# Kernel optimization log

Hardware: AMD Instinct MI355X
Metric: run time of the kernel (lower is better)

The kernel has to match this reference:

```python
import jax, jax.numpy as jnp
import numpy as np

M, N, DIM = 128, 128, 256
BS = 8192
START_SIGMA = max(M, N) / 2.0
EPOCHS = 20.0
START_LR = 0.5
TAU = EPOCHS / np.log(START_SIGMA)


def setup_inputs() -> dict:
    key = jax.random.key(0)
    k_data, k_w = jax.random.split(key)
    data = jax.random.normal(k_data, (BS, DIM), dtype=jnp.float32)
    all_weights = jax.random.normal(k_w, (M, N, DIM), dtype=jnp.float32)
    return {"data": data, "all_weights": all_weights, "it": 3}


def reference(data, all_weights, it):
    m, n, dim = all_weights.shape
    bs = data.shape[0]

    # decayed sigma and learning rate (scalar schedule)
    sigma = START_SIGMA * jnp.exp(-jnp.float32(it) / jnp.float32(TAU))
    lr = START_LR * jnp.exp(-jnp.float32(it) / jnp.float32(EPOCHS))

    # pairwise Euclidean distances: [bs, m*n]
    w_flat = all_weights.reshape(m * n, dim)
    x_sq = jnp.sum(data * data, axis=1, keepdims=True)            # [bs, 1]
    w_sq = jnp.sum(w_flat * w_flat, axis=1)[None, :]              # [1, m*n]
    dists = jnp.sqrt(x_sq + w_sq - 2.0 * data @ w_flat.T)         # [bs, m*n]

    # best-matching unit grid coordinates (unravel over (m, n))
    bmu = jnp.argmin(dists, axis=1)                               # [bs]
    wins0 = (bmu // n).astype(jnp.float32)                        # row coord
    wins1 = (bmu % n).astype(jnp.float32)                         # col coord

    # Gaussian neighborhood around BMU, scaled by lr: [bs, m, n]
    d = 2.0 * sigma * sigma
    rows = jnp.arange(m, dtype=jnp.float32)
    cols = jnp.arange(n, dtype=jnp.float32)
    px = jnp.exp(-(rows[None, :] - wins0[:, None]) ** 2 / d)      # [bs, m]
    py = jnp.exp(-(cols[None, :] - wins1[:, None]) ** 2 / d)      # [bs, n]
    neighbor = (px[:, :, None] * py[:, None, :]) * lr             # [bs, m, n]

    # weighted batch update of the codebook
    denom = jnp.sum(neighbor, axis=0)[..., None]                  # [m, n, 1]
    numer = jnp.einsum('bk,bd->kd', neighbor.reshape(bs, m * n), data)
    numer = numer.reshape(m, n, dim)                              # [m, n, dim]
    new_weights = jnp.where(denom != 0, numer / denom, all_weights)
    return new_weights
```

## Files before the change

kernel.cpp:

```cpp
#include <hip/hip_runtime.h>
#include <hip/hip_fp16.h>

#define BS    8192
#define DIM   256
#define KTOT  16384
#define CAND_CAP 131072
#define MARGIN 1.0f

typedef __attribute__((ext_vector_type(8))) _Float16 half8;
typedef __attribute__((ext_vector_type(4))) float f32x4;
typedef unsigned long long u64;

__device__ inline ushort f2h(float f) { return __half_as_ushort(__float2half(f)); }

__device__ inline void gload_lds16(const void* g, void* l) {
    __builtin_amdgcn_global_load_lds(
        (const __attribute__((address_space(1))) unsigned int*)g,
        (__attribute__((address_space(3))) unsigned int*)l, 16, 0, 0);
}

__device__ inline unsigned int fmap(float f) {
    unsigned int b = __float_as_uint(f);
    return (b & 0x80000000u) ? ~b : (b | 0x80000000u);
}
__device__ inline float unfmap(unsigned int m) {
    return (m & 0x80000000u) ? __uint_as_float(m & 0x7FFFFFFFu)
                             : __uint_as_float(~m);
}

__global__ void setup_all_kernel(float* __restrict__ S, float* __restrict__ G,
                                 float* __restrict__ cntf, unsigned int* __restrict__ keys,
                                 u64* __restrict__ keys2, unsigned int* __restrict__ cnt,
                                 const int* __restrict__ itp) {
    int idx = blockIdx.x * 256 + threadIdx.x;
    *(float4*)&S[(size_t)idx * 4] = make_float4(0.f, 0.f, 0.f, 0.f);
    if (idx < KTOT) {
        float itf = (float)itp[0];
        const float START_SIGMA = 64.0f;
        const float TAU = (float)(20.0 / 4.1588830833596715);
        float sigma = START_SIGMA * expf(-itf / TAU);
        float d2 = 2.0f * sigma * sigma;
        int i = idx >> 7, j = idx & 127;
        float diff = (float)(i - j);
        G[idx] = expf(-(diff * diff) / d2);
        cntf[idx] = 0.f;
    }
    if (idx < BS) { keys[idx] = 0xFFFFFFFFu; keys2[idx] = ~0ULL; }
    if (idx == 0) cnt[0] = 0u;
}

__global__ void cvt_all_kernel(const float* __restrict__ x, const float* __restrict__ w,
                               ushort* __restrict__ xf, ushort* __restrict__ wf,
                               float* __restrict__ wsq) {
    int wid = threadIdx.x >> 6, lane = threadIdx.x & 63;
    int row = blockIdx.x * 4 + wid;
    int h = lane * 4;
    int window = h >> 5, c = (h >> 3) & 3, off = h & 7;
    if (row < BS) {
        int swpos = (window << 5) + (((c ^ ((row >> 1) & 3)) << 3)) + off;
        float4 v = *(const float4*)&x[(size_t)row * DIM + h];
        ushort4 hv;
        hv.x = f2h(v.x); hv.y = f2h(v.y); hv.z = f2h(v.z); hv.w = f2h(v.w);
        *(ushort4*)&xf[(size_t)row * DIM + swpos] = hv;
    } else {
        int r = row - BS;
        int swpos = (window << 5) + (((c ^ ((r >> 1) & 3)) << 3)) + off;
        float4 v = *(const float4*)&w[(size_t)r * DIM + h];
        ushort4 hv;
        hv.x = f2h(v.x); hv.y = f2h(v.y); hv.z = f2h(v.z); hv.w = f2h(v.w);
        *(ushort4*)&wf[(size_t)r * DIM + swpos] = hv;
        float s = v.x * v.x + v.y * v.y + v.z * v.z + v.w * v.w;
        #pragma unroll
        for (int o = 32; o; o >>= 1) s += __shfl_down(s, o, 64);
        if (lane == 0) wsq[r] = s;
    }
}

__global__ __launch_bounds__(256) void bmu_pass1_kernel(
    const ushort* __restrict__ xf, const ushort* __restrict__ wf,
    const float* __restrict__ wsq, unsigned int* __restrict__ keys) {
    __shared__ ushort A[128 * 32];
    __shared__ ushort B[128 * 32];
    __shared__ float red[128][2];

    int m0 = blockIdx.x * 128;
    int kbase = blockIdx.y * 1024;
    int tid = threadIdx.x, w = tid >> 6, lane = tid & 63;
    int wm = (w & 1) * 64, wn = (w >> 1) * 64;
    int lm = lane & 15, quad = lane >> 4;
    int sw = (quad ^ ((lm >> 1) & 3)) * 8;
    int srow = lane >> 2, scol = (lane & 3) * 8;

    float best[4][4];
    #pragma unroll
    for (int mi = 0; mi < 4; ++mi)
        #pragma unroll
        for (int r = 0; r < 4; ++r) best[mi][r] = 3.4e38f;

    for (int kt = 0; kt < 8; ++kt) {
        int k0 = kbase + kt * 128;
        f32x4 acc[4][4];
        #pragma unroll
        for (int mi = 0; mi < 4; ++mi)
            #pragma unroll
            for (int ni = 0; ni < 4; ++ni)
                acc[mi][ni] = (f32x4){0.f, 0.f, 0.f, 0.f};

        for (int kb = 0; kb < DIM; kb += 32) {
            size_t axoff = (size_t)(m0 + w * 32 + srow) * DIM + kb + scol;
            size_t bxoff = (size_t)(k0 + w * 32 + srow) * DIM + kb + scol;
            gload_lds16(xf + axoff,            &A[(w * 32) * 32]);
            gload_lds16(xf + axoff + 16 * DIM, &A[(w * 32 + 16) * 32]);
            gload_lds16(wf + bxoff,            &B[(w * 32) * 32]);
            gload_lds16(wf + bxoff + 16 * DIM, &B[(w * 32 + 16) * 32]);
            __syncthreads();
            half8 av[4], bv[4];
            #pragma unroll
            for (int mi = 0; mi < 4; ++mi)
                av[mi] = *(const half8*)&A[(wm + mi * 16 + lm) * 32 + sw];
            #pragma unroll
            for (int ni = 0; ni < 4; ++ni)
                bv[ni] = *(const half8*)&B[(wn + ni * 16 + lm) * 32 + sw];
            #pragma unroll
            for (int mi = 0; mi < 4; ++mi)
                #pragma unroll
                for (int ni = 0; ni < 4; ++ni)
                    acc[mi][ni] = __builtin_amdgcn_mfma_f32_16x16x32_f16(
                        av[mi], bv[ni], acc[mi][ni], 0, 0, 0);
            __syncthreads();
        }
        float wsqv[4];
        #pragma unroll
        for (int ni = 0; ni < 4; ++ni) wsqv[ni] = wsq[k0 + wn + ni * 16 + lm];
        #pragma unroll
        for (int mi = 0; mi < 4; ++mi)
            #pragma unroll
            for (int r = 0; r < 4; ++r) {
                #pragma unroll
                for (int ni = 0; ni < 4; ++ni) {
                    float sc = fmaf(-2.0f, acc[mi][ni][r], wsqv[ni]);
                    best[mi][r] = fminf(best[mi][r], sc);
                }
            }
    }
    #pragma unroll
    for (int mi = 0; mi < 4; ++mi)
        #pragma unroll
        for (int r = 0; r < 4; ++r) {
            float b = best[mi][r];
            #pragma unroll
            for (int mask = 1; mask < 16; mask <<= 1)
                b = fminf(b, __shfl_xor(b, mask, 64));
            if (lm == 0) red[wm + mi * 16 + quad * 4 + r][w >> 1] = b;
        }
    __syncthreads();
    if (tid < 128) {
        float b = fminf(red[tid][0], red[tid][1]);
        atomicMin(&keys[m0 + tid], fmap(b));
    }
}

__global__ __launch_bounds__(256) void bmu_pass2_kernel(
    const ushort* __restrict__ xf, const ushort* __restrict__ wf,
    const float* __restrict__ wsq, const unsigned int* __restrict__ keys,
    u64* __restrict__ cand, unsigned int* __restrict__ cnt) {
    __shared__ ushort A[128 * 32];
    __shared__ ushort B[128 * 32];

    int m0 = blockIdx.x * 128;
    int kbase = blockIdx.y * 1024;
    int tid = threadIdx.x, w = tid >> 6, lane = tid & 63;
    int wm = (w & 1) * 64, wn = (w >> 1) * 64;
    int lm = lane & 15, quad = lane >> 4;
    int sw = (quad ^ ((lm >> 1) & 3)) * 8;
    int srow = lane >> 2, scol = (lane & 3) * 8;

    float thr[4][4];
    #pragma unroll
    for (int mi = 0; mi < 4; ++mi)
        #pragma unroll
        for (int r = 0; r < 4; ++r)
            thr[mi][r] = unfmap(keys[m0 + wm + mi * 16 + quad * 4 + r]) + MARGIN;

    for (int kt = 0; kt < 8; ++kt) {
        int k0 = kbase + kt * 128;
        f32x4 acc[4][4];
        #pragma unroll
        for (int mi = 0; mi < 4; ++mi)
            #pragma unroll
            for (int ni = 0; ni < 4; ++ni)
                acc[mi][ni] = (f32x4){0.f, 0.f, 0.f, 0.f};

        for (int kb = 0; kb < DIM; kb += 32) {
            size_t axoff = (size_t)(m0 + w * 32 + srow) * DIM + kb + scol;
            size_t bxoff = (size_t)(k0 + w * 32 + srow) * DIM + kb + scol;
            gload_lds16(xf + axoff,            &A[(w * 32) * 32]);
            gload_lds16(xf + axoff + 16 * DIM, &A[(w * 32 + 16) * 32]);
            gload_lds16(wf + bxoff,            &B[(w * 32) * 32]);
            gload_lds16(wf + bxoff + 16 * DIM, &B[(w * 32 + 16) * 32]);
            __syncthreads();
            half8 av[4], bv[4];
            #pragma unroll
            for (int mi = 0; mi < 4; ++mi)
                av[mi] = *(const half8*)&A[(wm + mi * 16 + lm) * 32 + sw];
            #pragma unroll
            for (int ni = 0; ni < 4; ++ni)
                bv[ni] = *(const half8*)&B[(wn + ni * 16 + lm) * 32 + sw];
            #pragma unroll
            for (int mi = 0; mi < 4; ++mi)
                #pragma unroll
                for (int ni = 0; ni < 4; ++ni)
                    acc[mi][ni] = __builtin_amdgcn_mfma_f32_16x16x32_f16(
                        av[mi], bv[ni], acc[mi][ni], 0, 0, 0);
            __syncthreads();
        }
        float wsqv[4];
        #pragma unroll
        for (int ni = 0; ni < 4; ++ni) wsqv[ni] = wsq[k0 + wn + ni * 16 + lm];
        #pragma unroll
        for (int mi = 0; mi < 4; ++mi)
            #pragma unroll
            for (int r = 0; r < 4; ++r) {
                int s = m0 + wm + mi * 16 + quad * 4 + r;
                #pragma unroll
                for (int ni = 0; ni < 4; ++ni) {
                    float sc = fmaf(-2.0f, acc[mi][ni][r], wsqv[ni]);
                    if (sc <= thr[mi][r]) {
                        unsigned int idx = atomicAdd(cnt, 1u);
                        if (idx < CAND_CAP)
                            cand[idx] = ((u64)(unsigned int)s << 32) |
                                        (unsigned int)(k0 + wn + ni * 16 + lm);
                    }
                }
            }
    }
}

__global__ __launch_bounds__(256) void bmu_refine_kernel(
    const float* __restrict__ x, const float* __restrict__ w,
    const u64* __restrict__ cand, const unsigned int* __restrict__ cnt,
    u64* __restrict__ keys2) {
    int lane = threadIdx.x & 63;
    int wid = blockIdx.x * 4 + (threadIdx.x >> 6);
    unsigned int n = cnt[0];
    if (n > CAND_CAP) n = CAND_CAP;
    for (unsigned int c = wid; c < n; c += 256 * 4) {
        u64 e = cand[c];
        unsigned int s = (unsigned int)(e >> 32);
        unsigned int k = (unsigned int)e;
        float4 xv = *(const float4*)&x[(size_t)s * DIM + lane * 4];
        float4 wv = *(const float4*)&w[(size_t)k * DIM + lane * 4];
        float dx = xv.x - wv.x, dy = xv.y - wv.y;
        float dz = xv.z - wv.z, dw = xv.w - wv.w;
        float d = dx * dx + dy * dy + dz * dz + dw * dw;
        #pragma unroll
        for (int off = 32; off; off >>= 1) d += __shfl_down(d, off, 64);
        if (lane == 0)
            atomicMin(&keys2[s], ((u64)fmap(d) << 32) | k);
    }
}

__global__ __launch_bounds__(256) void scatter_kernel(
    const float* __restrict__ x, const u64* __restrict__ keys2,
    float* __restrict__ S, float* __restrict__ cntf) {
    int lane = threadIdx.x & 63;
    int s = blockIdx.x * 4 + (threadIdx.x >> 6);
    unsigned int k = (unsigned int)keys2[s];
    float4 xv = *(const float4*)&x[(size_t)s * DIM + lane * 4];
    float* Sp = &S[(size_t)k * DIM + lane * 4];
    atomicAdd(Sp + 0, xv.x);
    atomicAdd(Sp + 1, xv.y);
    atomicAdd(Sp + 2, xv.z);
    atomicAdd(Sp + 3, xv.w);
    if (lane == 0) atomicAdd(&cntf[k], 1.0f);
}

__global__ __launch_bounds__(256) void gemm1_kernel(
    const float* __restrict__ G, const float* __restrict__ S, float* __restrict__ T) {
    __shared__ float Sl[128 * 68];
    int n0 = blockIdx.x * 64;
    int tid = threadIdx.x;
    #pragma unroll
    for (int q = 0; q < 8; ++q) {
        int idx = q * 256 + tid;
        int row = idx >> 4, c4 = (idx & 15) * 4;
        *(float4*)&Sl[row * 68 + c4] = *(const float4*)&S[(size_t)row * 32768 + n0 + c4];
    }
    __syncthreads();
    int ng = tid & 15, ig = tid >> 4;
    for (int pass = 0; pass < 2; ++pass) {
        int ibase = pass * 64 + ig * 4;
        float acc[4][4] = {};
        for (int a = 0; a < 128; ++a) {
            float4 sv = *(const float4*)&Sl[a * 68 + ng * 4];
            #pragma unroll
            for (int ii = 0; ii < 4; ++ii) {
                float g = G[(ibase + ii) * 128 + a];
                acc[ii][0] = fmaf(g, sv.x, acc[ii][0]);
                acc[ii][1] = fmaf(g, sv.y, acc[ii][1]);
                acc[ii][2] = fmaf(g, sv.z, acc[ii][2]);
                acc[ii][3] = fmaf(g, sv.w, acc[ii][3]);
            }
        }
        #pragma unroll
        for (int ii = 0; ii < 4; ++ii)
            *(float4*)&T[(size_t)(ibase + ii) * 32768 + n0 + ng * 4] =
                *(float4*)&acc[ii][0];
    }
}

__global__ void denom_s1_kernel(const float* __restrict__ cntf, const float* __restrict__ G,
                                float* __restrict__ M1) {
    int a = blockIdx.x, j = threadIdx.x;
    float acc = 0.f;
    for (int b2 = 0; b2 < 128; ++b2)
        acc = fmaf(cntf[a * 128 + b2], G[b2 * 128 + j], acc);
    M1[a * 128 + j] = acc;
}

__global__ void denom_s2_kernel(const float* __restrict__ G, const float* __restrict__ M1,
                                float* __restrict__ denom) {
    int i = blockIdx.x, j = threadIdx.x;
    float acc = 0.f;
    for (int a = 0; a < 128; ++a)
        acc = fmaf(G[i * 128 + a], M1[a * 128 + j], acc);
    denom[i * 128 + j] = acc;
}

__global__ __launch_bounds__(256) void gemm2_fin_kernel(
    const float* __restrict__ G, const float* __restrict__ T,
    const float* __restrict__ denom, const float* __restrict__ w,
    float* __restrict__ out) {
    __shared__ float Tl[128 * 68];
    int i = blockIdx.x, dq = blockIdx.y;
    int tid = threadIdx.x;
    #pragma unroll
    for (int q = 0; q < 8; ++q) {
        int idx = q * 256 + tid;
        int row = idx >> 4, c4 = (idx & 15) * 4;
        *(float4*)&Tl[row * 68 + c4] =
            *(const float4*)&T[(size_t)i * 32768 + row * 256 + dq * 64 + c4];
    }
    __syncthreads();
    int dg = tid & 15, jg = tid >> 4;
    for (int pass = 0; pass < 2; ++pass) {
        int jbase = pass * 64 + jg * 4;
        float acc[4][4] = {};
        for (int b2 = 0; b2 < 128; ++b2) {
            float4 tv = *(const float4*)&Tl[b2 * 68 + dg * 4];
            #pragma unroll
            for (int jj = 0; jj < 4; ++jj) {
                float g = G[(jbase + jj) * 128 + b2];
                acc[jj][0] = fmaf(g, tv.x, acc[jj][0]);
                acc[jj][1] = fmaf(g, tv.y, acc[jj][1]);
                acc[jj][2] = fmaf(g, tv.z, acc[jj][2]);
                acc[jj][3] = fmaf(g, tv.w, acc[jj][3]);
            }
        }
        #pragma unroll
        for (int jj = 0; jj < 4; ++jj) {
            int j = jbase + jj;
            float dv = denom[i * 128 + j];
            size_t e = (size_t)(i * 128 + j) * DIM + dq * 64 + dg * 4;
            float4 r;
            if (dv != 0.0f) {
                float inv = 1.0f / dv;
                r.x = acc[jj][0] * inv; r.y = acc[jj][1] * inv;
                r.z = acc[jj][2] * inv; r.w = acc[jj][3] * inv;
            } else {
                r = *(const float4*)&w[e];
            }
            *(float4*)&out[e] = r;
        }
    }
}

extern "C" void kernel_launch(void* const* d_in, const int* in_sizes, int n_in,
                              void* d_out, int out_size, void* d_ws, size_t ws_size,
                              hipStream_t stream) {
    const float* data = (const float*)d_in[0];
    const float* w    = (const float*)d_in[1];
    const int*   itp  = (const int*)d_in[2];
    float* out = (float*)d_out;

    char* ws = (char*)d_ws;
    size_t off = 0;
    float*        wsq   = (float*)(ws + off);        off += 65536;
    unsigned int* keys  = (unsigned int*)(ws + off); off += 65536;
    u64*          keys2 = (u64*)(ws + off);          off += 65536;
    unsigned int* cnt   = (unsigned int*)(ws + off); off += 65536;
    float*        G     = (float*)(ws + off);        off += 65536;
    float*        cntf  = (float*)(ws + off);        off += 65536;
    float*        M1    = (float*)(ws + off);        off += 65536;
    float*        denom = (float*)(ws + off);        off += 65536;
    ushort*       xf    = (ushort*)(ws + off);       off += 4194304;
    ushort*       wf    = (ushort*)(ws + off);       off += 8388608;
    u64*          cand  = (u64*)(ws + off);          off += 1048576;
    float*        S     = (float*)(ws + off);        off += 16777216;
    float*        T     = (float*)(ws + off);        off += 16777216;

    setup_all_kernel<<<4096, 256, 0, stream>>>(S, G, cntf, keys, keys2, cnt, itp);
    cvt_all_kernel<<<(BS + KTOT) / 4, 256, 0, stream>>>(data, w, xf, wf, wsq);
    bmu_pass1_kernel<<<dim3(64, 16), 256, 0, stream>>>(xf, wf, wsq, keys);
    bmu_pass2_kernel<<<dim3(64, 16), 256, 0, stream>>>(xf, wf, wsq, keys, cand, cnt);
    bmu_refine_kernel<<<256, 256, 0, stream>>>(data, w, cand, cnt, keys2);
    scatter_kernel<<<BS / 4, 256, 0, stream>>>(data, keys2, S, cntf);
    gemm1_kernel<<<512, 256, 0, stream>>>(G, S, T);
    denom_s1_kernel<<<128, 128, 0, stream>>>(cntf, G, M1);
    denom_s2_kernel<<<128, 128, 0, stream>>>(G, M1, denom);
    gemm2_fin_kernel<<<dim3(128, 4), 256, 0, stream>>>(G, T, denom, w, out);
}
```

Before: 402.6 us.

## Replace two-pass BMU GEMM with single scan storing quantized per-lane minima

The two full fp16 distance GEMM passes (one for the min threshold, one to collect candidates) become a single scan. The scan writes a byte-quantized minimum for each group of four codebook columns into a 32MB buffer. A collect kernel finds each sample's quantized minimum and emits group tasks within a small margin, and a rescore kernel evaluates the 4 columns of each group exactly in fp32. The goal is to drop one of the two GEMM passes; the cost is extra global traffic for the byte buffer, a fixed quantization scale and offset that assume a particular score range, and a changed k-split grid (12 splits over 128 tiles).

Result: slower. 516.7 us (+28.4%).

```diff
diff --git a/kernel.cpp b/kernel.cpp
--- a/kernel.cpp
+++ b/kernel.cpp
@@ -4,8 +4,7 @@
 #define BS    8192
 #define DIM   256
 #define KTOT  16384
-#define CAND_CAP 131072
-#define MARGIN 1.0f
+#define TASK_CAP 131072
 
 typedef __attribute__((ext_vector_type(8))) _Float16 half8;
 typedef __attribute__((ext_vector_type(4))) float f32x4;
@@ -23,15 +22,10 @@
     unsigned int b = __float_as_uint(f);
     return (b & 0x80000000u) ? ~b : (b | 0x80000000u);
 }
-__device__ inline float unfmap(unsigned int m) {
-    return (m & 0x80000000u) ? __uint_as_float(m & 0x7FFFFFFFu)
-                             : __uint_as_float(~m);
-}
 
 __global__ void setup_all_kernel(float* __restrict__ S, float* __restrict__ G,
-                                 float* __restrict__ cntf, unsigned int* __restrict__ keys,
-                                 u64* __restrict__ keys2, unsigned int* __restrict__ cnt,
-                                 const int* __restrict__ itp) {
+                                 float* __restrict__ cntf, u64* __restrict__ keys2,
+                                 unsigned int* __restrict__ cnt, const int* __restrict__ itp) {
     int idx = blockIdx.x * 256 + threadIdx.x;
     *(float4*)&S[(size_t)idx * 4] = make_float4(0.f, 0.f, 0.f, 0.f);
     if (idx < KTOT) {
@@ -45,7 +39,7 @@
         G[idx] = expf(-(diff * diff) / d2);
         cntf[idx] = 0.f;
     }
-    if (idx < BS) { keys[idx] = 0xFFFFFFFFu; keys2[idx] = ~0ULL; }
+    if (idx < BS) keys2[idx] = ~0ULL;
     if (idx == 0) cnt[0] = 0u;
 }
 
@@ -57,14 +51,14 @@
     int h = lane * 4;
     int window = h >> 5, c = (h >> 3) & 3, off = h & 7;
     if (row < BS) {
-        int swpos = (window << 5) + (((c ^ ((row >> 1) & 3)) << 3)) + off;
+        int swpos = (window << 5) + ((c ^ ((row >> 1) & 3)) << 3) + off;
         float4 v = *(const float4*)&x[(size_t)row * DIM + h];
         ushort4 hv;
         hv.x = f2h(v.x); hv.y = f2h(v.y); hv.z = f2h(v.z); hv.w = f2h(v.w);
         *(ushort4*)&xf[(size_t)row * DIM + swpos] = hv;
     } else {
         int r = row - BS;
-        int swpos = (window << 5) + (((c ^ ((r >> 1) & 3)) << 3)) + off;
+        int swpos = (window << 5) + ((c ^ ((r >> 1) & 3)) << 3) + off;
         float4 v = *(const float4*)&w[(size_t)r * DIM + h];
         ushort4 hv;
         hv.x = f2h(v.x); hv.y = f2h(v.y); hv.z = f2h(v.z); hv.w = f2h(v.w);
@@ -76,29 +70,25 @@
     }
 }
 
-__global__ __launch_bounds__(256) void bmu_pass1_kernel(
+__global__ __launch_bounds__(256, 3) void bmu_scan_kernel(
     const ushort* __restrict__ xf, const ushort* __restrict__ wf,
-    const float* __restrict__ wsq, unsigned int* __restrict__ keys) {
+    const float* __restrict__ wsq, unsigned char* __restrict__ laneMin) {
     __shared__ ushort A[128 * 32];
     __shared__ ushort B[128 * 32];
-    __shared__ float red[128][2];
 
     int m0 = blockIdx.x * 128;
-    int kbase = blockIdx.y * 1024;
+    int ksplit = blockIdx.y;
     int tid = threadIdx.x, w = tid >> 6, lane = tid & 63;
-    int wm = (w & 1) * 64, wn = (w >> 1) * 64;
+    int wm = (w & 1) * 64;
+    int wnIdx = w >> 1, wn = wnIdx * 64;
     int lm = lane & 15, quad = lane >> 4;
     int sw = (quad ^ ((lm >> 1) & 3)) * 8;
     int srow = lane >> 2, scol = (lane & 3) * 8;
 
-    float best[4][4];
-    #pragma unroll
-    for (int mi = 0; mi < 4; ++mi)
-        #pragma unroll
-        for (int r = 0; r < 4; ++r) best[mi][r] = 3.4e38f;
-
-    for (int kt = 0; kt < 8; ++kt) {
-        int k0 = kbase + kt * 128;
+    for (int kt = 0; kt < 11; ++kt) {
+        int tile = kt * 12 + ksplit;
+        if (tile >= 128) break;
+        int k0 = tile * 128;
         f32x4 acc[4][4];
         #pragma unroll
         for (int mi = 0; mi < 4; ++mi)
@@ -132,131 +122,86 @@
         float wsqv[4];
         #pragma unroll
         for (int ni = 0; ni < 4; ++ni) wsqv[ni] = wsq[k0 + wn + ni * 16 + lm];
-        #pragma unroll
-        for (int mi = 0; mi < 4; ++mi)
+        size_t baseA = ((size_t)(tile * 2 + wnIdx) * 8192 + m0 + wm + quad * 4) * 16 + lm;
+        #pragma unroll
+        for (int mi = 0; mi < 4; ++mi) {
             #pragma unroll
             for (int r = 0; r < 4; ++r) {
-                #pragma unroll
-                for (int ni = 0; ni < 4; ++ni) {
-                    float sc = fmaf(-2.0f, acc[mi][ni][r], wsqv[ni]);
-                    best[mi][r] = fminf(best[mi][r], sc);
-                }
+                float s0 = fmaf(-2.0f, acc[mi][0][r], wsqv[0]);
+                float s1 = fmaf(-2.0f, acc[mi][1][r], wsqv[1]);
+                float s2 = fmaf(-2.0f, acc[mi][2][r], wsqv[2]);
+                float s3 = fmaf(-2.0f, acc[mi][3][r], wsqv[3]);
+                float m = fminf(fminf(s0, s1), fminf(s2, s3));
+                float qf = fminf(fmaxf(rintf(fmaf(m, 0.33333334f, 100.0f)), 0.f), 255.f);
+                laneMin[baseA + (size_t)(mi * 16 + r) * 16] = (unsigned char)(int)qf;
             }
+        }
+    }
+}
+
+__global__ __launch_bounds__(256) void collect_kernel(
+    const unsigned char* __restrict__ laneMin, unsigned int* __restrict__ tasks,
+    unsigned int* __restrict__ cnt) {
+    int tid = threadIdx.x;
+    int sl = tid >> 4, lm = tid & 15;
+    int s = blockIdx.x * 16 + sl;
+    int qmin = 255;
+    #pragma unroll 4
+    for (int t = 0; t < 256; ++t) {
+        int v = laneMin[((size_t)t * 8192 + s) * 16 + lm];
+        qmin = v < qmin ? v : qmin;
     }
     #pragma unroll
-    for (int mi = 0; mi < 4; ++mi)
-        #pragma unroll
-        for (int r = 0; r < 4; ++r) {
-            float b = best[mi][r];
-            #pragma unroll
-            for (int mask = 1; mask < 16; mask <<= 1)
-                b = fminf(b, __shfl_xor(b, mask, 64));
-            if (lm == 0) red[wm + mi * 16 + quad * 4 + r][w >> 1] = b;
-        }
-    __syncthreads();
-    if (tid < 128) {
-        float b = fminf(red[tid][0], red[tid][1]);
-        atomicMin(&keys[m0 + tid], fmap(b));
-    }
-}
-
-__global__ __launch_bounds__(256) void bmu_pass2_kernel(
-    const ushort* __restrict__ xf, const ushort* __restrict__ wf,
-    const float* __restrict__ wsq, const unsigned int* __restrict__ keys,
-    u64* __restrict__ cand, unsigned int* __restrict__ cnt) {
-    __shared__ ushort A[128 * 32];
-    __shared__ ushort B[128 * 32];
-
-    int m0 = blockIdx.x * 128;
-    int kbase = blockIdx.y * 1024;
-    int tid = threadIdx.x, w = tid >> 6, lane = tid & 63;
-    int wm = (w & 1) * 64, wn = (w >> 1) * 64;
-    int lm = lane & 15, quad = lane >> 4;
-    int sw = (quad ^ ((lm >> 1) & 3)) * 8;
-    int srow = lane >> 2, scol = (lane & 3) * 8;
-
-    float thr[4][4];
-    #pragma unroll
-    for (int mi = 0; mi < 4; ++mi)
-        #pragma unroll
-        for (int r = 0; r < 4; ++r)
-            thr[mi][r] = unfmap(keys[m0 + wm + mi * 16 + quad * 4 + r]) + MARGIN;
-
-    for (int kt = 0; kt < 8; ++kt) {
-        int k0 = kbase + kt * 128;
-        f32x4 acc[4][4];
-        #pragma unroll
-        for (int mi = 0; mi < 4; ++mi)
-            #pragma unroll
-            for (int ni = 0; ni < 4; ++ni)
-                acc[mi][ni] = (f32x4){0.f, 0.f, 0.f, 0.f};
-
-        for (int kb = 0; kb < DIM; kb += 32) {
-            size_t axoff = (size_t)(m0 + w * 32 + srow) * DIM + kb + scol;
-            size_t bxoff = (size_t)(k0 + w * 32 + srow) * DIM + kb + scol;
-            gload_lds16(xf + axoff,            &A[(w * 32) * 32]);
-            gload_lds16(xf + axoff + 16 * DIM, &A[(w * 32 + 16) * 32]);
-            gload_lds16(wf + bxoff,            &B[(w * 32) * 32]);
-            gload_lds16(wf + bxoff + 16 * DIM, &B[(w * 32 + 16) * 32]);
-            __syncthreads();
-            half8 av[4], bv[4];
-            #pragma unroll
-            for (int mi = 0; mi < 4; ++mi)
-                av[mi] = *(const half8*)&A[(wm + mi * 16 + lm) * 32 + sw];
-            #pragma unroll
-            for (int ni = 0; ni < 4; ++ni)
-                bv[ni] = *(const half8*)&B[(wn + ni * 16 + lm) * 32 + sw];
-            #pragma unroll
-            for (int mi = 0; mi < 4; ++mi)
-                #pragma unroll
-                for (int ni = 0; ni < 4; ++ni)
-                    acc[mi][ni] = __builtin_amdgcn_mfma_f32_16x16x32_f16(
-                        av[mi], bv[ni], acc[mi][ni], 0, 0, 0);
-            __syncthreads();
-        }
-        float wsqv[4];
-        #pragma unroll
-        for (int ni = 0; ni < 4; ++ni) wsqv[ni] = wsq[k0 + wn + ni * 16 + lm];
-        #pragma unroll
-        for (int mi = 0; mi < 4; ++mi)
-            #pragma unroll
-            for (int r = 0; r < 4; ++r) {
-                int s = m0 + wm + mi * 16 + quad * 4 + r;
-                #pragma unroll
-                for (int ni = 0; ni < 4; ++ni) {
-                    float sc = fmaf(-2.0f, acc[mi][ni][r], wsqv[ni]);
-                    if (sc <= thr[mi][r]) {
-                        unsigned int idx = atomicAdd(cnt, 1u);
-                        if (idx < CAND_CAP)
-                            cand[idx] = ((u64)(unsigned int)s << 32) |
-                                        (unsigned int)(k0 + wn + ni * 16 + lm);
-                    }
-                }
-            }
-    }
-}
-
-__global__ __launch_bounds__(256) void bmu_refine_kernel(
+    for (int mask = 1; mask < 16; mask <<= 1) {
+        int o = __shfl_xor(qmin, mask, 64);
+        qmin = o < qmin ? o : qmin;
+    }
+    int thr = qmin + 2;
+    #pragma unroll 4
+    for (int t = 0; t < 256; ++t) {
+        int v = laneMin[((size_t)t * 8192 + s) * 16 + lm];
+        if (v <= thr) {
+            unsigned int idx = atomicAdd(cnt, 1u);
+            if (idx < TASK_CAP)
+                tasks[idx] = ((unsigned int)s << 12) | ((unsigned int)t << 4) | (unsigned int)lm;
+        }
+    }
+}
+
+__global__ __launch_bounds__(256) void rescore_kernel(
     const float* __restrict__ x, const float* __restrict__ w,
-    const u64* __restrict__ cand, const unsigned int* __restrict__ cnt,
+    const unsigned int* __restrict__ tasks, const unsigned int* __restrict__ cnt,
     u64* __restrict__ keys2) {
-    int lane = threadIdx.x & 63;
-    int wid = blockIdx.x * 4 + (threadIdx.x >> 6);
+    int tid = threadIdx.x;
+    int lane = tid & 63;
+    int gw = (blockIdx.x * 256 + tid) >> 6;
     unsigned int n = cnt[0];
-    if (n > CAND_CAP) n = CAND_CAP;
-    for (unsigned int c = wid; c < n; c += 256 * 4) {
-        u64 e = cand[c];
-        unsigned int s = (unsigned int)(e >> 32);
-        unsigned int k = (unsigned int)e;
-        float4 xv = *(const float4*)&x[(size_t)s * DIM + lane * 4];
-        float4 wv = *(const float4*)&w[(size_t)k * DIM + lane * 4];
-        float dx = xv.x - wv.x, dy = xv.y - wv.y;
-        float dz = xv.z - wv.z, dw = xv.w - wv.w;
-        float d = dx * dx + dy * dy + dz * dz + dw * dw;
-        #pragma unroll
-        for (int off = 32; off; off >>= 1) d += __shfl_down(d, off, 64);
-        if (lane == 0)
-            atomicMin(&keys2[s], ((u64)fmap(d) << 32) | k);
+    if (n > TASK_CAP) n = TASK_CAP;
+    int g = lane >> 4, l16 = lane & 15;
+    for (unsigned int t = gw; t < n; t += 256 * 4) {
+        unsigned int v = tasks[t];
+        int lmv = v & 15;
+        int tw = (v >> 4) & 255;
+        int s = v >> 12;
+        int wn = tw & 1, tile = tw >> 1;
+        int k = tile * 128 + wn * 64 + g * 16 + lmv;
+        float dist = 0.f;
+        #pragma unroll
+        for (int j = 0; j < 4; ++j) {
+            int d = j * 64 + l16 * 4;
+            float4 xv = *(const float4*)&x[(size_t)s * DIM + d];
+            float4 wv = *(const float4*)&w[(size_t)k * DIM + d];
+            float dx = xv.x - wv.x, dy = xv.y - wv.y;
+            float dz = xv.z - wv.z, dw = xv.w - wv.w;
+            dist += dx * dx + dy * dy + dz * dz + dw * dw;
+        }
+        #pragma unroll
+        for (int mask = 1; mask < 16; mask <<= 1)
+            dist += __shfl_xor(dist, mask, 64);
+        u64 p = ((u64)fmap(dist) << 32) | (unsigned int)k;
+        u64 o = __shfl_xor(p, 16, 64); p = o < p ? o : p;
+        o = __shfl_xor(p, 32, 64);     p = o < p ? o : p;
+        if (lane == 0) atomicMin(&keys2[s], p);
     }
 }
 
@@ -385,25 +330,25 @@
 
     char* ws = (char*)d_ws;
     size_t off = 0;
-    float*        wsq   = (float*)(ws + off);        off += 65536;
-    unsigned int* keys  = (unsigned int*)(ws + off); off += 65536;
-    u64*          keys2 = (u64*)(ws + off);          off += 65536;
-    unsigned int* cnt   = (unsigned int*)(ws + off); off += 65536;
-    float*        G     = (float*)(ws + off);        off += 65536;
-    float*        cntf  = (float*)(ws + off);        off += 65536;
-    float*        M1    = (float*)(ws + off);        off += 65536;
-    float*        denom = (float*)(ws + off);        off += 65536;
-    ushort*       xf    = (ushort*)(ws + off);       off += 4194304;
-    ushort*       wf    = (ushort*)(ws + off);       off += 8388608;
-    u64*          cand  = (u64*)(ws + off);          off += 1048576;
-    float*        S     = (float*)(ws + off);        off += 16777216;
-    float*        T     = (float*)(ws + off);        off += 16777216;
-
-    setup_all_kernel<<<4096, 256, 0, stream>>>(S, G, cntf, keys, keys2, cnt, itp);
+    float*         wsq     = (float*)(ws + off);         off += 65536;
+    u64*           keys2   = (u64*)(ws + off);           off += 65536;
+    unsigned int*  cnt     = (unsigned int*)(ws + off);  off += 65536;
+    float*         G       = (float*)(ws + off);         off += 65536;
+    float*         cntf    = (float*)(ws + off);         off += 65536;
+    float*         M1      = (float*)(ws + off);         off += 65536;
+    float*         denom   = (float*)(ws + off);         off += 65536;
+    ushort*        xf      = (ushort*)(ws + off);        off += 4194304;
+    ushort*        wf      = (ushort*)(ws + off);        off += 8388608;
+    unsigned int*  tasks   = (unsigned int*)(ws + off);  off += 1048576;
+    float*         S       = (float*)(ws + off);         off += 16777216;
+    unsigned char* laneMin = (unsigned char*)(ws + off); off += 33554432;
+    float*         T       = (float*)laneMin;
+
+    setup_all_kernel<<<4096, 256, 0, stream>>>(S, G, cntf, keys2, cnt, itp);
     cvt_all_kernel<<<(BS + KTOT) / 4, 256, 0, stream>>>(data, w, xf, wf, wsq);
-    bmu_pass1_kernel<<<dim3(64, 16), 256, 0, stream>>>(xf, wf, wsq, keys);
-    bmu_pass2_kernel<<<dim3(64, 16), 256, 0, stream>>>(xf, wf, wsq, keys, cand, cnt);
-    bmu_refine_kernel<<<256, 256, 0, stream>>>(data, w, cand, cnt, keys2);
+    bmu_scan_kernel<<<dim3(64, 12), 256, 0, stream>>>(xf, wf, wsq, laneMin);
+    collect_kernel<<<512, 256, 0, stream>>>(laneMin, tasks, cnt);
+    rescore_kernel<<<256, 256, 0, stream>>>(data, w, tasks, cnt, keys2);
     scatter_kernel<<<BS / 4, 256, 0, stream>>>(data, keys2, S, cntf);
     gemm1_kernel<<<512, 256, 0, stream>>>(G, S, T);
     denom_s1_kernel<<<128, 128, 0, stream>>>(cntf, G, M1);
```
